# Performance work log

Hardware: AMD Instinct MI355X
Metric: run time of the kernel (lower is better)

Reference implementation:

```python
import jax, jax.numpy as jnp
import numpy as np

N = 100000      # points
M = 12500       # cluster centers
E0 = 1600000    # point-level edges
E1 = 400000     # cluster-level edges
F_IN = 4        # raw point feature dim (e.g. intensity + extras)
D = 64          # hidden feature width
N_CLASSES = 8


def setup_inputs() -> dict:
    key = jax.random.key(0)
    ks = jax.random.split(key, 20)
    s = 0.05
    d = {}
    d["features"] = jax.random.normal(ks[0], (N, F_IN), jnp.float32)
    d["points"] = jax.random.normal(ks[1], (N, 3), jnp.float32)
    d["cluster_centers"] = jax.random.normal(ks[2], (M, 3), jnp.float32)
    d["l0_edges"] = jax.random.randint(ks[3], (E0, 2), 0, N)
    d["l1_edges"] = jax.random.randint(ks[4], (E1, 2), 0, M)
    d["labels"] = jax.random.randint(ks[5], (N,), 0, M)
    # Feature_extract MLP
    d["W_fe"] = s * jax.random.normal(ks[6], (F_IN + 3, D), jnp.float32)
    d["b_fe"] = jnp.zeros((D,), jnp.float32)
    # 4 Mini_GNN layers (layer2, layer2_1, layer6, layer6_1), stacked
    d["mini_We"] = s * jax.random.normal(ks[7], (4, D + 3, D), jnp.float32)
    d["mini_be"] = jnp.zeros((4, D), jnp.float32)
    d["mini_Wu"] = s * jax.random.normal(ks[8], (4, D, D), jnp.float32)
    d["mini_bu"] = jnp.zeros((4, D), jnp.float32)
    # Mini_to_Large
    d["W_m1"] = s * jax.random.normal(ks[9], (D + 3, D), jnp.float32)
    d["b_m1"] = jnp.zeros((D,), jnp.float32)
    d["W_m2"] = s * jax.random.normal(ks[10], (D, D), jnp.float32)
    d["b_m2"] = jnp.zeros((D,), jnp.float32)
    # 2 GNN layers on cluster graph (layer4, layer4_1), stacked
    d["gnn_We"] = s * jax.random.normal(ks[11], (2, D + 3, D), jnp.float32)
    d["gnn_be"] = jnp.zeros((2, D), jnp.float32)
    d["gnn_Wu"] = s * jax.random.normal(ks[12], (2, D, D), jnp.float32)
    d["gnn_bu"] = jnp.zeros((2, D), jnp.float32)
    # Large_to_Mini
    d["W_l"] = s * jax.random.normal(ks[13], (D + 3, D), jnp.float32)
    d["b_l"] = jnp.zeros((D,), jnp.float32)
    # Classifier
    d["W_c"] = s * jax.random.normal(ks[14], (D, N_CLASSES), jnp.float32)
    d["b_c"] = jnp.zeros((N_CLASSES,), jnp.float32)
    return d


def _gnn_layer(feat, pos, edges, We, be, Wu, bu, n_nodes):
    """PointGNN-style layer: gather -> edge MLP -> scatter max -> update MLP -> residual."""
    src, dst = edges[:, 0], edges[:, 1]
    e_in = jnp.concatenate([pos[src] - pos[dst], feat[src]], axis=-1)  # [E, 3+D]
    h = jax.nn.relu(e_in @ We + be)                                     # [E, D]
    agg = jax.ops.segment_max(h, dst, num_segments=n_nodes)            # [n, D]
    agg = jnp.where(jnp.isneginf(agg), 0.0, agg)  # nodes with no in-edges -> 0
    return jax.nn.relu(agg @ Wu + bu) + feat


def reference(features, points, cluster_centers, l0_edges, l1_edges, labels,
              W_fe, b_fe, mini_We, mini_be, mini_Wu, mini_bu,
              W_m1, b_m1, W_m2, b_m2, gnn_We, gnn_be, gnn_Wu, gnn_bu,
              W_l, b_l, W_c, b_c):
    rel = points - cluster_centers[labels]  # [N, 3] point pos relative to its cluster
    # layer1: Feature_extract
    f1 = jax.nn.relu(jnp.concatenate([features, rel], -1) @ W_fe + b_fe)
    # layer2 / layer2_1: Mini_GNN (scatter max) on point graph
    f2 = _gnn_layer(f1, points, l0_edges, mini_We[0], mini_be[0], mini_Wu[0], mini_bu[0], N)
    f2_1 = _gnn_layer(f2, points, l0_edges, mini_We[1], mini_be[1], mini_Wu[1], mini_bu[1], N)
    # layer3: Mini_to_Large (scatter sum by labels)
    h = jax.nn.relu(jnp.concatenate([f2_1, rel], -1) @ W_m1 + b_m1)
    c = jax.ops.segment_sum(h, labels, num_segments=M)  # [M, D]
    f3 = jax.nn.relu(c @ W_m2 + b_m2)
    # layer4 / layer4_1: GNN (scatter max) on cluster graph
    f4 = _gnn_layer(f3, cluster_centers, l1_edges, gnn_We[0], gnn_be[0], gnn_Wu[0], gnn_bu[0], M)
    f4_1 = _gnn_layer(f4, cluster_centers, l1_edges, gnn_We[1], gnn_be[1], gnn_Wu[1], gnn_bu[1], M)
    # layer5: Large_to_Mini (gather by labels)
    f5 = jax.nn.relu(jnp.concatenate([f4_1[labels], rel], -1) @ W_l + b_l)
    # layer6 / layer6_1 with residual skips per call()
    f6 = _gnn_layer(f5, points, l0_edges, mini_We[2], mini_be[2], mini_Wu[2], mini_bu[2], N)
    f6 = f6 + f2_1
    f6_1 = _gnn_layer(f6, points, l0_edges, mini_We[3], mini_be[3], mini_Wu[3], mini_bu[3], N)
    final = f6_1 + f2
    return final @ W_c + b_c  # [N, N_CLASSES] per-point logits
```

## Files before the change

### kernel.cpp

```cpp
#include <hip/hip_runtime.h>


#define N_PTS   100000
#define M_CL    12500
#define E0_N    1600000
#define E1_N    400000

#define NB      256
#define BIN_CAP 16
#define RANGE0  391
#define RANGE1  49
#define BCAP0   8192
#define BCAP1   2048
#define BCAPL   1024

#define LSTR    72

typedef unsigned short ushortT;
typedef short  short8 __attribute__((ext_vector_type(8)));
typedef short  s4v    __attribute__((ext_vector_type(4)));
typedef float  v4f    __attribute__((ext_vector_type(4)));
typedef _Float16 h2   __attribute__((ext_vector_type(2)));
typedef unsigned u4v  __attribute__((ext_vector_type(4)));

__device__ inline ushortT f2bf(float x){
  union{float f; unsigned u;} v; v.f = x;
  unsigned r = v.u + 0x7fffu + ((v.u >> 16) & 1u);
  return (ushortT)(r >> 16);
}
__device__ inline float bf2f(ushortT h){
  union{unsigned u; float f;} v; v.u = ((unsigned)h) << 16;
  return v.f;
}
__device__ inline ushortT f2h(float x){
  union{_Float16 h; ushortT u;} v; v.h = (_Float16)x;
  return v.u;
}
__device__ inline float h2f(ushortT u){
  union{ushortT u; _Float16 h;} v; v.u = u;
  return (float)v.h;
}
__device__ inline h2 pkmax(h2 a, h2 b){ return __builtin_elementwise_max(a, b); }
__device__ inline h2 u2h(unsigned u){ union{unsigned u; h2 h;} v{u}; return v.h; }


struct WSrc { const float* p[22]; };

__global__ __launch_bounds__(256) void k_init_wprep(WSrc s, ushortT* __restrict__ wt, ushortT* __restrict__ wtc,
                                                    float* __restrict__ wpp,
                                                    int* c0, int* c1, int* cL){
  int blk = blockIdx.x;
  if (blk == 0){
    int t = threadIdx.x;
    c0[t] = t*BCAP0; c1[t] = t*BCAP1; cL[t] = t*BCAPL;
    return;
  }
  int slot = blk - 1;
  if (slot < 15){
    const float* src = s.p[slot];
    ushortT* dst = wt + slot*4096;
    for (int e=threadIdx.x; e<4096; e+=256){
      int nn = e>>6, p = e&63;
      int kk = (p&3)*16 + (p>>2);
      dst[e] = f2bf(src[kk*64+nn]);
    }
  } else if (slot == 15){
    const float* src = s.p[15];
    for (int e=threadIdx.x; e<1024; e+=256){
      int nn = e>>6, p = e&63;
      int kk = (p&3)*16 + (p>>2);
      wtc[e] = (nn<8) ? f2bf(src[kk*8+nn]) : (ushortT)0;
    }
  } else {
    for (int e=threadIdx.x; e<6*192; e+=256){
      int i = e/192, rem = e - i*192, r = rem>>6, p = rem&63;
      wpp[e] = s.p[16+i][r*64 + ((p&3)*16 + (p>>2))];
    }
  }
}


template<int RANGE, bool LAB>
__device__ void bin_seg(const int* __restrict__ edges, int E,
                        int* __restrict__ bcur, unsigned* __restrict__ tmp,
                        int bid, int nblk,
                        unsigned* stage, int* scnt, int* sbase){
  int tid = threadIdx.x;
  int nchunks = (E + 2047) / 2048;
  for (int c = bid; c < nchunks; c += nblk){
    int base = c*2048;
    scnt[tid] = 0;
    __syncthreads();
    #pragma unroll
    for (int r=0;r<8;++r){
      int e = base + r*256 + tid;
      if (e < E){
        int s, d;
        if (LAB){ s = e; d = edges[e]; }
        else    { int2 ed = ((const int2*)edges)[e]; s = ed.x; d = ed.y; }
        int bk = d / RANGE;
        unsigned packed = ((unsigned)s << 11) | (unsigned)(d - bk*RANGE);
        int pos = atomicAdd(&scnt[bk], 1);
        if (pos < BIN_CAP) stage[bk*BIN_CAP+pos] = packed;
        else tmp[atomicAdd(&bcur[bk],1)] = packed;
      }
    }
    __syncthreads();
    {
      int nfl = scnt[tid]; if (nfl > BIN_CAP) nfl = BIN_CAP;
      sbase[tid] = atomicAdd(&bcur[tid], nfl);
    }
    __syncthreads();
    int wv = tid >> 6, ln = tid & 63;
    for (int bb=0; bb<16; ++bb){
      int bk = wv*64 + bb*4 + (ln>>4);
      int ent = ln & 15;
      int nf = scnt[bk]; if (nf > BIN_CAP) nf = BIN_CAP;
      if (ent < nf) tmp[sbase[bk]+ent] = stage[bk*BIN_CAP+ent];
    }
    __syncthreads();
  }
}

template<int RANGE, int BCAP, int K>
__device__ void csr_build_seg(const unsigned* __restrict__ tmp, const int* __restrict__ bcur,
                              int n, int* __restrict__ offs, int* __restrict__ csr,
                              int b, int* hist, int* part){
  int tid = threadIdx.x;
  int dlo = b*RANGE;
  int range = n - dlo; if (range > RANGE) range = RANGE; if (range < 0) range = 0;
  int cnt = bcur[b] - b*BCAP;
  part[tid] = bcur[tid] - tid*BCAP;
  __syncthreads();
  for (int st=1; st<256; st<<=1){
    int x = (tid >= st) ? part[tid-st] : 0;
    __syncthreads();
    part[tid] += x;
    __syncthreads();
  }
  int gb = part[b] - cnt;
  int total = part[NB-1];
  if (b == NB-1 && tid == 0) offs[n] = total;
  __syncthreads();
  for (int t=tid; t<RANGE; t+=256) hist[t] = 0;
  __syncthreads();
  const unsigned* sl = tmp + (size_t)b*BCAP;
  for (int j=tid; j<cnt; j+=256) atomicAdd(&hist[sl[j] & 2047u], 1);
  __syncthreads();
  int s = 0; int loc[K];
  #pragma unroll
  for (int kk=0; kk<K; ++kk){
    int idx = tid*K + kk;
    int v = (idx < RANGE) ? hist[idx] : 0;
    loc[kk] = s; s += v;
  }
  part[tid] = s; __syncthreads();
  int own = s;
  for (int st=1; st<256; st<<=1){
    int x = (tid >= st) ? part[tid-st] : 0;
    __syncthreads();
    part[tid] += x;
    __syncthreads();
  }
  int ebase = part[tid] - own;
  __syncthreads();
  #pragma unroll
  for (int kk=0; kk<K; ++kk){
    int idx = tid*K + kk;
    if (idx < RANGE){
      int ex = ebase + loc[kk];
      if (idx < range) offs[dlo+idx] = gb + ex;
      hist[idx] = ex;
    }
  }
  __syncthreads();
  for (int j=tid; j<cnt; j+=256){
    unsigned p = sl[j];
    int pos = atomicAdd(&hist[p & 2047u], 1);
    csr[gb + pos] = (int)(p >> 11);
  }
}

__global__ __launch_bounds__(256) void k_build_all(
    const unsigned* t0, const int* bc0, int* offs0, int* csr0,
    const unsigned* t1, const int* bc1, int* offs1, int* csr1,
    const unsigned* tL, const int* bcL, int* offsL, int* csrL){
  __shared__ int hist[RANGE0];
  __shared__ int part[256];
  int b = blockIdx.x;
  if (b < 256)      csr_build_seg<RANGE0,BCAP0,2>(t0, bc0, N_PTS, offs0, csr0, b, hist, part);
  else if (b < 512) csr_build_seg<RANGE1,BCAP1,1>(t1, bc1, M_CL, offs1, csr1, b-256, hist, part);
  else              csr_build_seg<RANGE1,BCAPL,1>(tL, bcL, M_CL, offsL, csrL, b-512, hist, part);
}


__global__ __launch_bounds__(256) void k_bin_f1g(
    const int* __restrict__ l0e, const int* __restrict__ l1e, const int* __restrict__ labels,
    int* bc0, int* bc1, int* bcL,
    unsigned* t0, unsigned* t1, unsigned* tL,
    const float* __restrict__ features, const float* __restrict__ points,
    const float* __restrict__ centers,
    const float* __restrict__ W, const float* __restrict__ bfe,
    const ushortT* __restrict__ Wt2, const float* __restrict__ bias2,
    const float* __restrict__ Wr2,
    float* __restrict__ rel, ushortT* __restrict__ f1b,
    ushortT* __restrict__ gout, int n, int ntiles, int nf1blk)
{
  __shared__ char smem[18432];
  int b = blockIdx.x;
  if (b < 1027){
    unsigned* stage = (unsigned*)smem;
    int* scnt = (int*)(smem + 16384);
    int* sbase = (int*)(smem + 17408);
    if (b < 782)      bin_seg<RANGE0,false>(l0e, E0_N, bc0, t0, b, 782, stage, scnt, sbase);
    else if (b < 978) bin_seg<RANGE1,false>(l1e, E1_N, bc1, t1, b-782, 196, stage, scnt, sbase);
    else              bin_seg<RANGE1,true >(labels, N_PTS, bcL, tL, b-978, 49, stage, scnt, sbase);
    return;
  }
  ushortT* lds = (ushortT*)smem;
  int bb = b - 1027;
  int tid = threadIdx.x;
  int lane = tid & 63, wslot = tid >> 6;
  int quad = lane >> 4, l15 = lane & 15;
  int permL = (lane & 15)*4 + (lane >> 4);
  int r3 = lane/3, c3 = lane - r3*3;
  int gw = (bb*256 + tid) >> 6;
  int nw = (nf1blk*256) >> 6;
  float Wf0=W[0*64+lane], Wf1=W[1*64+lane], Wf2=W[2*64+lane], Wf3=W[3*64+lane];
  float wr0=W[4*64+lane], wr1=W[5*64+lane], wr2=W[6*64+lane];
  float bias=bfe[lane];
  short8 s0_0 = *(const short8*)(Wt2 + ( 0 + l15)*64 +  0 + quad*8);
  short8 s0_1 = *(const short8*)(Wt2 + ( 0 + l15)*64 + 32 + quad*8);
  short8 s1_0 = *(const short8*)(Wt2 + (16 + l15)*64 +  0 + quad*8);
  short8 s1_1 = *(const short8*)(Wt2 + (16 + l15)*64 + 32 + quad*8);
  short8 s2_0 = *(const short8*)(Wt2 + (32 + l15)*64 +  0 + quad*8);
  short8 s2_1 = *(const short8*)(Wt2 + (32 + l15)*64 + 32 + quad*8);
  short8 s3_0 = *(const short8*)(Wt2 + (48 + l15)*64 +  0 + quad*8);
  short8 s3_1 = *(const short8*)(Wt2 + (48 + l15)*64 + 32 + quad*8);
  float eb0 = bias2[l15], eb1 = bias2[16+l15], eb2 = bias2[32+l15], eb3 = bias2[48+l15];
  float e0c0=Wr2[0*64+l15], e0c1=Wr2[0*64+16+l15], e0c2=Wr2[0*64+32+l15], e0c3=Wr2[0*64+48+l15];
  float e1c0=Wr2[1*64+l15], e1c1=Wr2[1*64+16+l15], e1c2=Wr2[1*64+32+l15], e1c3=Wr2[1*64+48+l15];
  float e2c0=Wr2[2*64+l15], e2c1=Wr2[2*64+16+l15], e2c2=Wr2[2*64+32+l15], e2c3=Wr2[2*64+48+l15];

  for (int t=gw; t<ntiles; t+=nw){
    int i0 = t*16;
    int lab16 = labels[min(i0 + (lane & 15), n-1)];
    float fv  = features[(size_t)min(i0 + (lane>>2), n-1)*4 + (lane & 3)];
    int lb = __shfl(lab16, (r3 < 16) ? r3 : 0, 64);
    float pv = 0.f, relv = 0.f;
    if (lane < 48){
      int rowp = i0 + r3;
      int rc = (rowp < n) ? rowp : (n-1);
      pv = points[(size_t)rc*3 + c3];
      float cv = centers[(size_t)lb*3 + c3];
      relv = pv - cv;
      if (rowp < n) rel[(size_t)rowp*3 + c3] = relv;
    }
    #pragma unroll
    for (int r=0;r<16;++r){
      float rx = __shfl(relv, 3*r+0, 64);
      float ry = __shfl(relv, 3*r+1, 64);
      float rz = __shfl(relv, 3*r+2, 64);
      float f0 = __shfl(fv, 4*r+0, 64);
      float f1 = __shfl(fv, 4*r+1, 64);
      float f2 = __shfl(fv, 4*r+2, 64);
      float f3 = __shfl(fv, 4*r+3, 64);
      float acc = bias + wr0*rx + wr1*ry + wr2*rz;
      acc += f0*Wf0 + f1*Wf1;
      acc += f2*Wf2 + f3*Wf3;
      acc = fmaxf(acc, 0.f);
      ushortT ab = f2bf(acc);
      int row = i0 + r;
      if (row < n) f1b[(size_t)row*64 + permL] = ab;
      lds[wslot*(16*LSTR) + r*LSTR + permL] = ab;
    }
    __builtin_amdgcn_wave_barrier();
    const ushortT* lp = lds + wslot*(16*LSTR) + l15*LSTR + quad*8;
    short8 sa0 = *(const short8*)(lp);
    short8 sa1 = *(const short8*)(lp + 32);
    __builtin_amdgcn_wave_barrier();
    v4f ec0 = {0.f,0.f,0.f,0.f}, ec1 = ec0, ec2 = ec0, ec3 = ec0;
    ec0 = __builtin_amdgcn_mfma_f32_16x16x32_bf16(sa0, s0_0, ec0, 0,0,0);
    ec1 = __builtin_amdgcn_mfma_f32_16x16x32_bf16(sa0, s1_0, ec1, 0,0,0);
    ec2 = __builtin_amdgcn_mfma_f32_16x16x32_bf16(sa0, s2_0, ec2, 0,0,0);
    ec3 = __builtin_amdgcn_mfma_f32_16x16x32_bf16(sa0, s3_0, ec3, 0,0,0);
    ec0 = __builtin_amdgcn_mfma_f32_16x16x32_bf16(sa1, s0_1, ec0, 0,0,0);
    ec1 = __builtin_amdgcn_mfma_f32_16x16x32_bf16(sa1, s1_1, ec1, 0,0,0);
    ec2 = __builtin_amdgcn_mfma_f32_16x16x32_bf16(sa1, s2_1, ec2, 0,0,0);
    ec3 = __builtin_amdgcn_mfma_f32_16x16x32_bf16(sa1, s3_1, ec3, 0,0,0);
    #pragma unroll
    for (int r=0;r<4;++r){
      int row = i0 + quad*4 + r;
      if (row < n){
        int rr4 = quad*4 + r;
        float vx = __shfl(pv, 3*rr4+0, 64);
        float vy = __shfl(pv, 3*rr4+1, 64);
        float vz = __shfl(pv, 3*rr4+2, 64);
        float g0 = ec0[r] + eb0 + vx*e0c0 + vy*e1c0 + vz*e2c0;
        float g1 = ec1[r] + eb1 + vx*e0c1 + vy*e1c1 + vz*e2c1;
        float g2 = ec2[r] + eb2 + vx*e0c2 + vy*e1c2 + vz*e2c2;
        float g3 = ec3[r] + eb3 + vx*e0c3 + vy*e1c3 + vz*e2c3;
        s4v o; o.x=(short)f2h(g0); o.y=(short)f2h(g1); o.z=(short)f2h(g2); o.w=(short)f2h(g3);
        *(s4v*)(gout + (size_t)row*64 + l15*4) = o;
      }
    }
  }
}


template<bool RELU, int NRES, bool USEREL, bool GATHER, bool OUT16, bool F16O, int EMODE, bool ERELU>
__global__ __launch_bounds__(256) void k_gemm(
    const ushortT* __restrict__ A, const ushortT* __restrict__ Wt,
    const float* __restrict__ bias, const float* __restrict__ Wr,
    const float* __restrict__ rel, const int* __restrict__ gidx,
    const ushortT* __restrict__ r1, const ushortT* __restrict__ r2,
    ushortT* __restrict__ out16,
    const ushortT* __restrict__ Wt2, const float* __restrict__ bias2,
    const float* __restrict__ Wr2, const float* __restrict__ vec2,
    void* __restrict__ eout,
    int n, int ntiles)
{
  constexpr int LDSZ = (EMODE>0) ? 4*16*LSTR : 4;
  __shared__ ushortT lds[LDSZ];
  int tid = threadIdx.x;
  int lane = tid & 63, wslot = tid >> 6;
  int quad = lane >> 4, l15 = lane & 15;
  int r3 = lane/3, c3 = lane - r3*3;
  int gw = (blockIdx.x*256 + tid) >> 6;
  int nw = (gridDim.x*256) >> 6;

  short8 bfr0_0 = *(const short8*)(Wt + ( 0 + l15)*64 +  0 + quad*8);
  short8 bfr0_1 = *(const short8*)(Wt + ( 0 + l15)*64 + 32 + quad*8);
  short8 bfr1_0 = *(const short8*)(Wt + (16 + l15)*64 +  0 + quad*8);
  short8 bfr1_1 = *(const short8*)(Wt + (16 + l15)*64 + 32 + quad*8);
  short8 bfr2_0 = *(const short8*)(Wt + (32 + l15)*64 +  0 + quad*8);
  short8 bfr2_1 = *(const short8*)(Wt + (32 + l15)*64 + 32 + quad*8);
  short8 bfr3_0 = *(const short8*)(Wt + (48 + l15)*64 +  0 + quad*8);
  short8 bfr3_1 = *(const short8*)(Wt + (48 + l15)*64 + 32 + quad*8);
  float bs0 = bias[ 0 + l15], bs1 = bias[16 + l15];
  float bs2 = bias[32 + l15], bs3 = bias[48 + l15];
  float w0c0=0,w0c1=0,w0c2=0,w0c3=0, w1c0=0,w1c1=0,w1c2=0,w1c3=0, w2c0=0,w2c1=0,w2c2=0,w2c3=0;
  if (USEREL){
    w0c0=Wr[0*64+l15]; w0c1=Wr[0*64+16+l15]; w0c2=Wr[0*64+32+l15]; w0c3=Wr[0*64+48+l15];
    w1c0=Wr[1*64+l15]; w1c1=Wr[1*64+16+l15]; w1c2=Wr[1*64+32+l15]; w1c3=Wr[1*64+48+l15];
    w2c0=Wr[2*64+l15]; w2c1=Wr[2*64+16+l15]; w2c2=Wr[2*64+32+l15]; w2c3=Wr[2*64+48+l15];
  }

  short8 s0_0{}, s0_1{}, s1_0{}, s1_1{}, s2_0{}, s2_1{}, s3_0{}, s3_1{};
  float eb0=0, eb1=0, eb2=0, eb3=0;
  float e0c0=0,e0c1=0,e0c2=0,e0c3=0, e1c0=0,e1c1=0,e1c2=0,e1c3=0, e2c0=0,e2c1=0,e2c2=0,e2c3=0;
  float ebias_c = 0.f;
  if (EMODE == 1){
    s0_0 = *(const short8*)(Wt2 + ( 0 + l15)*64 +  0 + quad*8);
    s0_1 = *(const short8*)(Wt2 + ( 0 + l15)*64 + 32 + quad*8);
    s1_0 = *(const short8*)(Wt2 + (16 + l15)*64 +  0 + quad*8);
    s1_1 = *(const short8*)(Wt2 + (16 + l15)*64 + 32 + quad*8);
    s2_0 = *(const short8*)(Wt2 + (32 + l15)*64 +  0 + quad*8);
    s2_1 = *(const short8*)(Wt2 + (32 + l15)*64 + 32 + quad*8);
    s3_0 = *(const short8*)(Wt2 + (48 + l15)*64 +  0 + quad*8);
    s3_1 = *(const short8*)(Wt2 + (48 + l15)*64 + 32 + quad*8);
    eb0 = bias2[l15]; eb1 = bias2[16+l15]; eb2 = bias2[32+l15]; eb3 = bias2[48+l15];
    e0c0=Wr2[0*64+l15]; e0c1=Wr2[0*64+16+l15]; e0c2=Wr2[0*64+32+l15]; e0c3=Wr2[0*64+48+l15];
    e1c0=Wr2[1*64+l15]; e1c1=Wr2[1*64+16+l15]; e1c2=Wr2[1*64+32+l15]; e1c3=Wr2[1*64+48+l15];
    e2c0=Wr2[2*64+l15]; e2c1=Wr2[2*64+16+l15]; e2c2=Wr2[2*64+32+l15]; e2c3=Wr2[2*64+48+l15];
  } else if (EMODE == 2){
    s0_0 = *(const short8*)(Wt2 + l15*64 +  0 + quad*8);
    s0_1 = *(const short8*)(Wt2 + l15*64 + 32 + quad*8);
    ebias_c = (l15 < 8) ? bias2[l15] : 0.f;
  }

  for (int t=gw; t<ntiles; t+=nw){
    int i0 = t*16;
    int rowA = i0 + l15; if (rowA >= n) rowA = n-1;
    if (GATHER) rowA = gidx[rowA];
    const ushortT* ap = A + (size_t)rowA*64 + quad*8;
    short8 a0 = *(const short8*)(ap);
    short8 a1 = *(const short8*)(ap + 32);
    float relL = 0.f;
    if (USEREL && lane < 48){
      int rc = i0 + r3; if (rc >= n) rc = n-1;
      relL = rel[(size_t)rc*3 + c3];
    }
    v4f ac0 = {0.f,0.f,0.f,0.f}, ac1 = ac0, ac2 = ac0, ac3 = ac0;
    ac0 = __builtin_amdgcn_mfma_f32_16x16x32_bf16(a0, bfr0_0, ac0, 0,0,0);
    ac1 = __builtin_amdgcn_mfma_f32_16x16x32_bf16(a0, bfr1_0, ac1, 0,0,0);
    ac2 = __builtin_amdgcn_mfma_f32_16x16x32_bf16(a0, bfr2_0, ac2, 0,0,0);
    ac3 = __builtin_amdgcn_mfma_f32_16x16x32_bf16(a0, bfr3_0, ac3, 0,0,0);
    ac0 = __builtin_amdgcn_mfma_f32_16x16x32_bf16(a1, bfr0_1, ac0, 0,0,0);
    ac1 = __builtin_amdgcn_mfma_f32_16x16x32_bf16(a1, bfr1_1, ac1, 0,0,0);
    ac2 = __builtin_amdgcn_mfma_f32_16x16x32_bf16(a1, bfr2_1, ac2, 0,0,0);
    ac3 = __builtin_amdgcn_mfma_f32_16x16x32_bf16(a1, bfr3_1, ac3, 0,0,0);

    #pragma unroll
    for (int r=0;r<4;++r){
      int row = i0 + quad*4 + r;
      bool rowok = (row < n);
      float v0 = ac0[r] + bs0, v1 = ac1[r] + bs1, v2 = ac2[r] + bs2, v3 = ac3[r] + bs3;
      if (USEREL){
        int rr4 = quad*4 + r;
        float rx = __shfl(relL, 3*rr4+0, 64);
        float ry = __shfl(relL, 3*rr4+1, 64);
        float rz = __shfl(relL, 3*rr4+2, 64);
        v0 += rx*w0c0 + ry*w1c0 + rz*w2c0;
        v1 += rx*w0c1 + ry*w1c1 + rz*w2c1;
        v2 += rx*w0c2 + ry*w1c2 + rz*w2c2;
        v3 += rx*w0c3 + ry*w1c3 + rz*w2c3;
      }
      if (RELU){ v0=fmaxf(v0,0.f); v1=fmaxf(v1,0.f); v2=fmaxf(v2,0.f); v3=fmaxf(v3,0.f); }
      size_t pb = (size_t)row*64 + l15*4;
      if (rowok){
        if (NRES>=1){
          s4v rv = *(const s4v*)(r1 + pb);
          v0 += bf2f((ushortT)rv.x); v1 += bf2f((ushortT)rv.y);
          v2 += bf2f((ushortT)rv.z); v3 += bf2f((ushortT)rv.w);
        }
        if (NRES>=2){
          s4v rv = *(const s4v*)(r2 + pb);
          v0 += bf2f((ushortT)rv.x); v1 += bf2f((ushortT)rv.y);
          v2 += bf2f((ushortT)rv.z); v3 += bf2f((ushortT)rv.w);
        }
        if (OUT16){
          s4v o;
          if (F16O){ o.x=(short)f2h(v0); o.y=(short)f2h(v1); o.z=(short)f2h(v2); o.w=(short)f2h(v3); }
          else     { o.x=(short)f2bf(v0); o.y=(short)f2bf(v1); o.z=(short)f2bf(v2); o.w=(short)f2bf(v3); }
          *(s4v*)(out16 + pb) = o;
        }
      }
      if (EMODE > 0){
        int lb = wslot*(16*LSTR) + (quad*4+r)*LSTR + l15*4;
        s4v o; o.x=(short)f2bf(v0); o.y=(short)f2bf(v1); o.z=(short)f2bf(v2); o.w=(short)f2bf(v3);
        *(s4v*)(lds + lb) = o;
      }
    }

    if (EMODE > 0){
      __builtin_amdgcn_wave_barrier();
      const ushortT* lp = lds + wslot*(16*LSTR) + l15*LSTR + quad*8;
      short8 sa0 = *(const short8*)(lp);
      short8 sa1 = *(const short8*)(lp + 32);
      __builtin_amdgcn_wave_barrier();
      if (EMODE == 1){
        float posv = 0.f;
        if (lane < 48){
          int rc = i0 + r3; if (rc >= n) rc = n-1;
          posv = vec2[(size_t)rc*3 + c3];
        }
        v4f ec0 = {0.f,0.f,0.f,0.f}, ec1 = ec0, ec2 = ec0, ec3 = ec0;
        ec0 = __builtin_amdgcn_mfma_f32_16x16x32_bf16(sa0, s0_0, ec0, 0,0,0);
        ec1 = __builtin_amdgcn_mfma_f32_16x16x32_bf16(sa0, s1_0, ec1, 0,0,0);
        ec2 = __builtin_amdgcn_mfma_f32_16x16x32_bf16(sa0, s2_0, ec2, 0,0,0);
        ec3 = __builtin_amdgcn_mfma_f32_16x16x32_bf16(sa0, s3_0, ec3, 0,0,0);
        ec0 = __builtin_amdgcn_mfma_f32_16x16x32_bf16(sa1, s0_1, ec0, 0,0,0);
        ec1 = __builtin_amdgcn_mfma_f32_16x16x32_bf16(sa1, s1_1, ec1, 0,0,0);
        ec2 = __builtin_amdgcn_mfma_f32_16x16x32_bf16(sa1, s2_1, ec2, 0,0,0);
        ec3 = __builtin_amdgcn_mfma_f32_16x16x32_bf16(sa1, s3_1, ec3, 0,0,0);
        ushortT* eo = (ushortT*)eout;
        #pragma unroll
        for (int r=0;r<4;++r){
          int row = i0 + quad*4 + r;
          if (row < n){
            int rr4 = quad*4 + r;
            float vx = __shfl(posv, 3*rr4+0, 64);
            float vy = __shfl(posv, 3*rr4+1, 64);
            float vz = __shfl(posv, 3*rr4+2, 64);
            float g0 = ec0[r] + eb0 + vx*e0c0 + vy*e1c0 + vz*e2c0;
            float g1 = ec1[r] + eb1 + vx*e0c1 + vy*e1c1 + vz*e2c1;
            float g2 = ec2[r] + eb2 + vx*e0c2 + vy*e1c2 + vz*e2c2;
            float g3 = ec3[r] + eb3 + vx*e0c3 + vy*e1c3 + vz*e2c3;
            if (ERELU){ g0=fmaxf(g0,0.f); g1=fmaxf(g1,0.f); g2=fmaxf(g2,0.f); g3=fmaxf(g3,0.f); }
            s4v o; o.x=(short)f2h(g0); o.y=(short)f2h(g1); o.z=(short)f2h(g2); o.w=(short)f2h(g3);
            *(s4v*)(eo + (size_t)row*64 + l15*4) = o;
          }
        }
      } else {
        v4f ec = {0.f,0.f,0.f,0.f};
        ec = __builtin_amdgcn_mfma_f32_16x16x32_bf16(sa0, s0_0, ec, 0,0,0);
        ec = __builtin_amdgcn_mfma_f32_16x16x32_bf16(sa1, s0_1, ec, 0,0,0);
        if (l15 < 8){
          float* eo = (float*)eout;
          #pragma unroll
          for (int r=0;r<4;++r){
            int row = i0 + quad*4 + r;
            if (row < n) eo[(size_t)row*8 + l15] = ec[r] + ebias_c;
          }
        }
      }
    }
  }
}


__global__ __launch_bounds__(256) void k_edge_agg(const int* __restrict__ offs, const int* __restrict__ csr,
                                                  const float* __restrict__ pos, const ushortT* __restrict__ g,
                                                  const float* __restrict__ Wp, ushortT* __restrict__ agg, int n){
  int lane = threadIdx.x & 63;
  int grp = lane >> 3, d8 = lane & 7;
  int gbase = lane & 56;
  int gw = (blockIdx.x*256 + threadIdx.x) >> 6;
  int nw = (gridDim.x*256) >> 6;
  const u4v* g4 = (const u4v*)g;
  float2 w0[4], w1[4], w2[4];
  #pragma unroll
  for (int q=0;q<4;++q){
    w0[q] = *(const float2*)(Wp + 0*64 + d8*8 + 2*q);
    w1[q] = *(const float2*)(Wp + 1*64 + d8*8 + 2*q);
    w2[q] = *(const float2*)(Wp + 2*64 + d8*8 + 2*q);
  }
  const h2 NEGBIG = {(_Float16)-60000.f, (_Float16)-60000.f};
  int n8 = (n+7) >> 3;
  for (int ii=gw; ii<n8; ii+=nw){
    int i0 = ii*8;
    int ig = i0 + grp; bool ok = ig < n; if (!ok) ig = n-1;
    int b = offs[ig], e = offs[ig+1];
    int cnt = e - b, c1 = cnt - 1;
    int mx = cnt;
    mx = max(mx, __shfl_xor(mx, 8, 64));
    mx = max(mx, __shfl_xor(mx, 16, 64));
    mx = max(mx, __shfl_xor(mx, 32, 64));
    h2 m0=NEGBIG, m1=NEGBIG, m2=NEGBIG, m3=NEGBIG;
    for (int J=0; J<mx; J+=8){
      if (J < cnt){
        int sv = csr[b + min(J + d8, c1)];
        #pragma unroll
        for (int jj=0; jj<8; ++jj){
          int s = __shfl(sv, gbase + jj, 64);
          u4v u = g4[(size_t)s*8 + d8];
          m0 = pkmax(m0, u2h(u.x));
          m1 = pkmax(m1, u2h(u.y));
          m2 = pkmax(m2, u2h(u.z));
          m3 = pkmax(m3, u2h(u.w));
        }
      }
    }
    float px = pos[ig*3+0], py = pos[ig*3+1], pz = pos[ig*3+2];
    u4v outv;
    {
      float sA = w0[0].x*px + w1[0].x*py + w2[0].x*pz;
      float sB = w0[0].y*px + w1[0].y*py + w2[0].y*pz;
      outv.x = (unsigned)f2bf(fmaxf((float)m0.x - sA, 0.f)) |
               ((unsigned)f2bf(fmaxf((float)m0.y - sB, 0.f)) << 16);
    }
    {
      float sA = w0[1].x*px + w1[1].x*py + w2[1].x*pz;
      float sB = w0[1].y*px + w1[1].y*py + w2[1].y*pz;
      outv.y = (unsigned)f2bf(fmaxf((float)m1.x - sA, 0.f)) |
               ((unsigned)f2bf(fmaxf((float)m1.y - sB, 0.f)) << 16);
    }
    {
      float sA = w0[2].x*px + w1[2].x*py + w2[2].x*pz;
      float sB = w0[2].y*px + w1[2].y*py + w2[2].y*pz;
      outv.z = (unsigned)f2bf(fmaxf((float)m2.x - sA, 0.f)) |
               ((unsigned)f2bf(fmaxf((float)m2.y - sB, 0.f)) << 16);
    }
    {
      float sA = w0[3].x*px + w1[3].x*py + w2[3].x*pz;
      float sB = w0[3].y*px + w1[3].y*py + w2[3].y*pz;
      outv.w = (unsigned)f2bf(fmaxf((float)m3.x - sA, 0.f)) |
               ((unsigned)f2bf(fmaxf((float)m3.y - sB, 0.f)) << 16);
    }
    if (ok) ((u4v*)agg)[(size_t)ig*8 + d8] = outv;
  }
}


__global__ __launch_bounds__(256) void k_seg_gather(const int* __restrict__ offs, const int* __restrict__ csr,
                                                    const ushortT* __restrict__ h, ushortT* __restrict__ c, int m){
  int lane = threadIdx.x & 63;
  int wv = (blockIdx.x*256 + threadIdx.x) >> 6;
  if (wv >= m) return;
  int b = offs[wv], e = offs[wv+1];
  float acc = 0.f;
  for (int k=b; k<e; ++k){
    int i = csr[k];
    acc += h2f(h[(size_t)i*64+lane]);
  }
  c[(size_t)wv*64+lane] = f2bf(acc);
}


extern "C" void kernel_launch(void* const* d_in, const int* in_sizes, int n_in,
                              void* d_out, int out_size, void* d_ws, size_t ws_size,
                              hipStream_t stream){
  const float* features = (const float*)d_in[0];
  const float* points   = (const float*)d_in[1];
  const float* centers  = (const float*)d_in[2];
  const int*   l0e      = (const int*)d_in[3];
  const int*   l1e      = (const int*)d_in[4];
  const int*   labels   = (const int*)d_in[5];
  const float* W_fe = (const float*)d_in[6];
  const float* b_fe = (const float*)d_in[7];
  const float* mWe  = (const float*)d_in[8];
  const float* mbe  = (const float*)d_in[9];
  const float* mWu  = (const float*)d_in[10];
  const float* mbu  = (const float*)d_in[11];
  const float* W_m1 = (const float*)d_in[12];
  const float* b_m1 = (const float*)d_in[13];
  const float* W_m2 = (const float*)d_in[14];
  const float* b_m2 = (const float*)d_in[15];
  const float* gWe  = (const float*)d_in[16];
  const float* gbe  = (const float*)d_in[17];
  const float* gWu  = (const float*)d_in[18];
  const float* gbu  = (const float*)d_in[19];
  const float* W_l  = (const float*)d_in[20];
  const float* b_l  = (const float*)d_in[21];
  const float* W_c  = (const float*)d_in[22];
  const float* b_c  = (const float*)d_in[23];
  float* out = (float*)d_out;

  char* w = (char*)d_ws;
  size_t off = 0;
  auto alloc = [&](size_t bytes)->void*{
    void* p = (void*)(w + off);
    off = (off + bytes + 255) & ~(size_t)255;
    return p;
  };
  float* rel  = (float*)alloc((size_t)N_PTS*3*4);
  ushortT* UF1 = (ushortT*)alloc((size_t)N_PTS*64*2);
  ushortT* UF2 = (ushortT*)alloc((size_t)N_PTS*64*2);
  ushortT* UF21= (ushortT*)alloc((size_t)N_PTS*64*2);
  ushortT* UF5 = (ushortT*)alloc((size_t)N_PTS*64*2);
  ushortT* UF6 = (ushortT*)alloc((size_t)N_PTS*64*2);
  ushortT* gbuf= (ushortT*)alloc((size_t)N_PTS*64*2);
  ushortT* abuf= (ushortT*)alloc((size_t)N_PTS*64*2);
  ushortT* cb_b= (ushortT*)alloc((size_t)M_CL*64*2);
  ushortT* UF3 = (ushortT*)alloc((size_t)M_CL*64*2);
  ushortT* UF4 = (ushortT*)alloc((size_t)M_CL*64*2);
  ushortT* cg_b= (ushortT*)alloc((size_t)M_CL*64*2);
  ushortT* cagg_b = (ushortT*)alloc((size_t)M_CL*64*2);
  ushortT* f41_b  = (ushortT*)alloc((size_t)M_CL*64*2);
  ushortT* wt  = (ushortT*)alloc((size_t)15*4096*2);
  ushortT* wtc = (ushortT*)alloc((size_t)1024*2);
  float* wpp = (float*)alloc((size_t)6*192*4);
  int* offs0 = (int*)alloc((size_t)(N_PTS+1)*4);
  int* csr0  = (int*)alloc((size_t)E0_N*4);
  int* offs1 = (int*)alloc((size_t)(M_CL+1)*4);
  int* csr1  = (int*)alloc((size_t)E1_N*4);
  int* offsL = (int*)alloc((size_t)(M_CL+1)*4);
  int* csrL  = (int*)alloc((size_t)N_PTS*4);
  unsigned* tmp0 = (unsigned*)alloc((size_t)NB*BCAP0*4);
  unsigned* tmp1 = (unsigned*)alloc((size_t)NB*BCAP1*4);
  unsigned* tmpL = (unsigned*)alloc((size_t)NB*BCAPL*4);
  int* bcur0 = (int*)alloc(NB*4);
  int* bcur1 = (int*)alloc(NB*4);
  int* bcurL = (int*)alloc(NB*4);
  (void)ws_size; (void)in_sizes; (void)n_in; (void)out_size;

  const int NT_N = (N_PTS+15)/16;
  const int NT_M = (M_CL +15)/16;
  const int GBG_N = 1563;
  const int GBG_M = 196;
  const int GB_N  = 3125;
  const int GB_BIN = 1027;

  WSrc ws{};
  ws.p[0]=mWu+0*4096; ws.p[1]=mWu+1*4096; ws.p[2]=mWu+2*4096; ws.p[3]=mWu+3*4096;
  ws.p[4]=W_m2; ws.p[5]=gWu+0*4096; ws.p[6]=gWu+1*4096;
  ws.p[7]=mWe+0*4288+192; ws.p[8]=mWe+1*4288+192; ws.p[9]=mWe+2*4288+192; ws.p[10]=mWe+3*4288+192;
  ws.p[11]=W_m1; ws.p[12]=W_l; ws.p[13]=gWe+0*4288+192; ws.p[14]=gWe+1*4288+192;
  ws.p[15]=W_c;
  ws.p[16]=mWe+0*4288; ws.p[17]=mWe+1*4288; ws.p[18]=mWe+2*4288; ws.p[19]=mWe+3*4288;
  ws.p[20]=gWe+0*4288; ws.p[21]=gWe+1*4288;
  k_init_wprep<<<18, 256, 0, stream>>>(ws, wt, wtc, wpp, bcur0, bcur1, bcurL);
  k_bin_f1g<<<GB_BIN + GBG_N, 256, 0, stream>>>(l0e, l1e, labels, bcur0, bcur1, bcurL, tmp0, tmp1, tmpL,
      features, points, centers, W_fe, b_fe,
      wt+7*4096, mbe+0, mWe+0*4288, rel, UF1, gbuf, N_PTS, NT_N, GBG_N);
  k_build_all<<<768, 256, 0, stream>>>(tmp0, bcur0, offs0, csr0,
                                       tmp1, bcur1, offs1, csr1,
                                       tmpL, bcurL, offsL, csrL);

  k_edge_agg<<<GB_N,256,0,stream>>>(offs0, csr0, points, gbuf, wpp+0*192, abuf, N_PTS);
  k_gemm<true,1,false,false,true,false,1,false><<<GBG_N,256,0,stream>>>(abuf, wt+0*4096, mbu+0,
      nullptr, nullptr, nullptr, UF1, nullptr, UF2,
      wt+8*4096, mbe+64, mWe+1*4288, points, gbuf, N_PTS, NT_N);
  k_edge_agg<<<GB_N,256,0,stream>>>(offs0, csr0, points, gbuf, wpp+1*192, abuf, N_PTS);
  k_gemm<true,1,false,false,true,false,1,true><<<GBG_N,256,0,stream>>>(abuf, wt+1*4096, mbu+64,
      nullptr, nullptr, nullptr, UF2, nullptr, UF21,
      wt+11*4096, b_m1, W_m1+4096, rel, gbuf, N_PTS, NT_N);
  k_seg_gather<<<(M_CL*64+255)/256, 256, 0, stream>>>(offsL, csrL, gbuf, cb_b, M_CL);
  k_gemm<true,0,false,false,true,false,1,false><<<GBG_M,256,0,stream>>>(cb_b, wt+4*4096, b_m2,
      nullptr, nullptr, nullptr, nullptr, nullptr, UF3,
      wt+13*4096, gbe+0, gWe+0*4288, centers, cg_b, M_CL, NT_M);
  k_edge_agg<<<GBG_M,256,0,stream>>>(offs1, csr1, centers, cg_b, wpp+4*192, cagg_b, M_CL);
  k_gemm<true,1,false,false,true,false,1,false><<<GBG_M,256,0,stream>>>(cagg_b, wt+5*4096, gbu+0,
      nullptr, nullptr, nullptr, UF3, nullptr, UF4,
      wt+14*4096, gbe+64, gWe+1*4288, centers, cg_b, M_CL, NT_M);
  k_edge_agg<<<GBG_M,256,0,stream>>>(offs1, csr1, centers, cg_b, wpp+5*192, cagg_b, M_CL);
  k_gemm<true,1,false,false,true,false,0,false><<<GBG_M,256,0,stream>>>(cagg_b, wt+6*4096, gbu+64,
      nullptr, nullptr, nullptr, UF4, nullptr, f41_b,
      nullptr, nullptr, nullptr, nullptr, nullptr, M_CL, NT_M);
  k_gemm<true,0,true,true,true,false,1,false><<<GBG_N,256,0,stream>>>(f41_b, wt+12*4096, b_l,
      W_l+4096, rel, labels, nullptr, nullptr, UF5,
      wt+9*4096, mbe+128, mWe+2*4288, points, gbuf, N_PTS, NT_N);
  k_edge_agg<<<GB_N,256,0,stream>>>(offs0, csr0, points, gbuf, wpp+2*192, abuf, N_PTS);
  k_gemm<true,2,false,false,true,false,1,false><<<GBG_N,256,0,stream>>>(abuf, wt+2*4096, mbu+128,
      nullptr, nullptr, nullptr, UF5, UF21, UF6,
      wt+10*4096, mbe+192, mWe+3*4288, points, gbuf, N_PTS, NT_N);
  k_edge_agg<<<GB_N,256,0,stream>>>(offs0, csr0, points, gbuf, wpp+3*192, abuf, N_PTS);
  k_gemm<true,2,false,false,false,false,2,false><<<GBG_N,256,0,stream>>>(abuf, wt+3*4096, mbu+192,
      nullptr, nullptr, nullptr, UF6, UF2, nullptr,
      wtc, b_c, nullptr, nullptr, out, N_PTS, NT_N);
}
```

Measured before the change: 458.2 us.

## Replace atomic global binning with per-chunk local sort and gather-based CSR build

```diff
diff --git a/kernel.cpp b/kernel.cpp
--- a/kernel.cpp
+++ b/kernel.cpp
@@ -7,12 +7,14 @@
 #define E1_N    400000
 
 #define NB      256
-#define BIN_CAP 16
 #define RANGE0  391
 #define RANGE1  49
-#define BCAP0   8192
-#define BCAP1   2048
-#define BCAPL   1024
+#define NCH0    782
+#define NCH1    196
+#define NCHL    49
+#define CAP0    7168
+#define CAP1    2048
+#define CAPL    768
 
 #define LSTR    72
 
@@ -48,11 +50,11 @@
 
 __global__ __launch_bounds__(256) void k_init_wprep(WSrc s, ushortT* __restrict__ wt, ushortT* __restrict__ wtc,
                                                     float* __restrict__ wpp,
-                                                    int* c0, int* c1, int* cL){
+                                                    int* b0, int* b1, int* bL){
   int blk = blockIdx.x;
   if (blk == 0){
     int t = threadIdx.x;
-    c0[t] = t*BCAP0; c1[t] = t*BCAP1; cL[t] = t*BCAPL;
+    b0[t] = 0; b1[t] = 0; bL[t] = 0;
     return;
   }
   int slot = blk - 1;
@@ -81,56 +83,70 @@
 
 
 template<int RANGE, bool LAB>
-__device__ void bin_seg(const int* __restrict__ edges, int E,
-                        int* __restrict__ bcur, unsigned* __restrict__ tmp,
-                        int bid, int nblk,
-                        unsigned* stage, int* scnt, int* sbase){
+__device__ void sort_chunk(const int* __restrict__ edges, int E, int c,
+                           unsigned* __restrict__ slab, int* __restrict__ offC,
+                           int* __restrict__ btot,
+                           unsigned* slds, int* hist, int* pfx){
   int tid = threadIdx.x;
-  int nchunks = (E + 2047) / 2048;
-  for (int c = bid; c < nchunks; c += nblk){
-    int base = c*2048;
-    scnt[tid] = 0;
+  int base = c*2048;
+  int cnt = E - base; if (cnt > 2048) cnt = 2048;
+  hist[tid] = 0;
+  __syncthreads();
+  int bk[8]; unsigned pk[8];
+  #pragma unroll
+  for (int r=0;r<8;++r){
+    int e = base + r*256 + tid;
+    bk[r] = -1; pk[r] = 0;
+    if (e < E){
+      int s, d;
+      if (LAB){ s = e; d = edges[e]; }
+      else    { int2 ed = ((const int2*)edges)[e]; s = ed.x; d = ed.y; }
+      int b = d / RANGE;
+      bk[r] = b;
+      pk[r] = ((unsigned)s << 11) | (unsigned)(d - b*RANGE);
+      atomicAdd(&hist[b], 1);
+    }
+  }
+  __syncthreads();
+  int own = hist[tid];
+  pfx[tid] = own;
+  __syncthreads();
+  for (int st=1; st<256; st<<=1){
+    int x = (tid >= st) ? pfx[tid-st] : 0;
     __syncthreads();
-    #pragma unroll
-    for (int r=0;r<8;++r){
-      int e = base + r*256 + tid;
-      if (e < E){
-        int s, d;
-        if (LAB){ s = e; d = edges[e]; }
-        else    { int2 ed = ((const int2*)edges)[e]; s = ed.x; d = ed.y; }
-        int bk = d / RANGE;
-        unsigned packed = ((unsigned)s << 11) | (unsigned)(d - bk*RANGE);
-        int pos = atomicAdd(&scnt[bk], 1);
-        if (pos < BIN_CAP) stage[bk*BIN_CAP+pos] = packed;
-        else tmp[atomicAdd(&bcur[bk],1)] = packed;
-      }
-    }
+    pfx[tid] += x;
     __syncthreads();
-    {
-      int nfl = scnt[tid]; if (nfl > BIN_CAP) nfl = BIN_CAP;
-      sbase[tid] = atomicAdd(&bcur[tid], nfl);
-    }
-    __syncthreads();
-    int wv = tid >> 6, ln = tid & 63;
-    for (int bb=0; bb<16; ++bb){
-      int bk = wv*64 + bb*4 + (ln>>4);
-      int ent = ln & 15;
-      int nf = scnt[bk]; if (nf > BIN_CAP) nf = BIN_CAP;
-      if (ent < nf) tmp[sbase[bk]+ent] = stage[bk*BIN_CAP+ent];
-    }
-    __syncthreads();
-  }
-}
-
-template<int RANGE, int BCAP, int K>
-__device__ void csr_build_seg(const unsigned* __restrict__ tmp, const int* __restrict__ bcur,
+  }
+  int excl = pfx[tid] - own;
+  offC[(size_t)c*257 + tid] = excl;
+  if (tid == 0) offC[(size_t)c*257 + 256] = cnt;
+  atomicAdd(&btot[tid], own);
+  hist[tid] = excl;
+  __syncthreads();
+  #pragma unroll
+  for (int r=0;r<8;++r){
+    if (bk[r] >= 0){
+      int pos = atomicAdd(&hist[bk[r]], 1);
+      slds[pos] = pk[r];
+    }
+  }
+  __syncthreads();
+  unsigned* sg = slab + (size_t)c*2048;
+  for (int i=tid; i<cnt; i+=256) sg[i] = slds[i];
+}
+
+
+template<int RANGE, int NCHUNK, int CAP, int K>
+__device__ void csr_build_seg(const unsigned* __restrict__ slab, const int* __restrict__ offC,
+                              const int* __restrict__ btot,
                               int n, int* __restrict__ offs, int* __restrict__ csr,
-                              int b, int* hist, int* part){
+                              int b, unsigned* stage, int* hist, int* part){
+  constexpr int CPT = (NCHUNK + 255) / 256;
   int tid = threadIdx.x;
   int dlo = b*RANGE;
   int range = n - dlo; if (range > RANGE) range = RANGE; if (range < 0) range = 0;
-  int cnt = bcur[b] - b*BCAP;
-  part[tid] = bcur[tid] - tid*BCAP;
+  int ownT = btot[tid];
+  part[tid] = ownT;
   __syncthreads();
   for (int st=1; st<256; st<<=1){
     int x = (tid >= st) ? part[tid-st] : 0;
@@ -138,14 +154,46 @@
     part[tid] += x;
     __syncthreads();
   }
-  int gb = part[b] - cnt;
+  int gb = part[b] - btot[b];
   int total = part[NB-1];
   if (b == NB-1 && tid == 0) offs[n] = total;
+  int cnt = btot[b];
+  __syncthreads();
+  int mst[CPT], mlen[CPT];
+  int csum = 0;
+  #pragma unroll
+  for (int k=0;k<CPT;++k){
+    int c = tid + k*256;
+    int l = 0, s0 = 0;
+    if (c < NCHUNK){
+      s0 = offC[(size_t)c*257 + b];
+      l  = offC[(size_t)c*257 + b + 1] - s0;
+    }
+    mst[k] = s0; mlen[k] = l; csum += l;
+  }
+  part[tid] = csum;
+  __syncthreads();
+  int own2 = csum;
+  for (int st=1; st<256; st<<=1){
+    int x = (tid >= st) ? part[tid-st] : 0;
+    __syncthreads();
+    part[tid] += x;
+    __syncthreads();
+  }
+  int sb = part[tid] - own2;
+  #pragma unroll
+  for (int k=0;k<CPT;++k){
+    int c = tid + k*256;
+    if (c < NCHUNK){
+      const unsigned* sg = slab + (size_t)c*2048 + mst[k];
+      for (int j=0;j<mlen[k];++j) stage[sb+j] = sg[j];
+      sb += mlen[k];
+    }
+  }
   __syncthreads();
   for (int t=tid; t<RANGE; t+=256) hist[t] = 0;
   __syncthreads();
-  const unsigned* sl = tmp + (size_t)b*BCAP;
-  for (int j=tid; j<cnt; j+=256) atomicAdd(&hist[sl[j] & 2047u], 1);
+  for (int j=tid; j<cnt; j+=256) atomicAdd(&hist[stage[j] & 2047u], 1);
   __syncthreads();
   int s = 0; int loc[K];
   #pragma unroll
@@ -155,14 +203,14 @@
     loc[kk] = s; s += v;
   }
   part[tid] = s; __syncthreads();
-  int own = s;
+  int own3 = s;
   for (int st=1; st<256; st<<=1){
     int x = (tid >= st) ? part[tid-st] : 0;
     __syncthreads();
     part[tid] += x;
     __syncthreads();
   }
-  int ebase = part[tid] - own;
+  int ebase = part[tid] - own3;
   __syncthreads();
   #pragma unroll
   for (int kk=0; kk<K; ++kk){
@@ -175,29 +223,31 @@
   }
   __syncthreads();
   for (int j=tid; j<cnt; j+=256){
-    unsigned p = sl[j];
+    unsigned p = stage[j];
     int pos = atomicAdd(&hist[p & 2047u], 1);
     csr[gb + pos] = (int)(p >> 11);
   }
 }
 
 __global__ __launch_bounds__(256) void k_build_all(
-    const unsigned* t0, const int* bc0, int* offs0, int* csr0,
-    const unsigned* t1, const int* bc1, int* offs1, int* csr1,
-    const unsigned* tL, const int* bcL, int* offsL, int* csrL){
+    const unsigned* s0, const int* oc0, const int* bt0, int* offs0, int* csr0,
+    const unsigned* s1, const int* oc1, const int* bt1, int* offs1, int* csr1,
+    const unsigned* sL, const int* ocL, const int* btL, int* offsL, int* csrL){
+  __shared__ unsigned stage[CAP0];
   __shared__ int hist[RANGE0];
   __shared__ int part[256];
   int b = blockIdx.x;
-  if (b < 256)      csr_build_seg<RANGE0,BCAP0,2>(t0, bc0, N_PTS, offs0, csr0, b, hist, part);
-  else if (b < 512) csr_build_seg<RANGE1,BCAP1,1>(t1, bc1, M_CL, offs1, csr1, b-256, hist, part);
-  else              csr_build_seg<RANGE1,BCAPL,1>(tL, bcL, M_CL, offsL, csrL, b-512, hist, part);
+  if (b < 256)      csr_build_seg<RANGE0,NCH0,CAP0,2>(s0, oc0, bt0, N_PTS, offs0, csr0, b, stage, hist, part);
+  else if (b < 512) csr_build_seg<RANGE1,NCH1,CAP1,1>(s1, oc1, bt1, M_CL, offs1, csr1, b-256, stage, hist, part);
+  else              csr_build_seg<RANGE1,NCHL,CAPL,1>(sL, ocL, btL, M_CL, offsL, csrL, b-512, stage, hist, part);
 }
 
 
 __global__ __launch_bounds__(256) void k_bin_f1g(
     const int* __restrict__ l0e, const int* __restrict__ l1e, const int* __restrict__ labels,
-    int* bc0, int* bc1, int* bcL,
-    unsigned* t0, unsigned* t1, unsigned* tL,
+    int* bt0, int* bt1, int* btL,
+    unsigned* s0, unsigned* s1, unsigned* sL,
+    int* oc0, int* oc1, int* ocL,
     const float* __restrict__ features, const float* __restrict__ points,
     const float* __restrict__ centers,
     const float* __restrict__ W, const float* __restrict__ bfe,
@@ -206,15 +256,15 @@
     float* __restrict__ rel, ushortT* __restrict__ f1b,
     ushortT* __restrict__ gout, int n, int ntiles, int nf1blk)
 {
-  __shared__ char smem[18432];
+  __shared__ char smem[10240];
   int b = blockIdx.x;
   if (b < 1027){
-    unsigned* stage = (unsigned*)smem;
-    int* scnt = (int*)(smem + 16384);
-    int* sbase = (int*)(smem + 17408);
-    if (b < 782)      bin_seg<RANGE0,false>(l0e, E0_N, bc0, t0, b, 782, stage, scnt, sbase);
-    else if (b < 978) bin_seg<RANGE1,false>(l1e, E1_N, bc1, t1, b-782, 196, stage, scnt, sbase);
-    else              bin_seg<RANGE1,true >(labels, N_PTS, bcL, tL, b-978, 49, stage, scnt, sbase);
+    unsigned* slds = (unsigned*)smem;
+    int* hist = (int*)(smem + 8192);
+    int* pfx  = (int*)(smem + 9216);
+    if (b < 782)      sort_chunk<RANGE0,false>(l0e, E0_N, b,     s0, oc0, bt0, slds, hist, pfx);
+    else if (b < 978) sort_chunk<RANGE1,false>(l1e, E1_N, b-782, s1, oc1, bt1, slds, hist, pfx);
+    else              sort_chunk<RANGE1,true >(labels, N_PTS, b-978, sL, ocL, btL, slds, hist, pfx);
     return;
   }
   ushortT* lds = (ushortT*)smem;
@@ -637,12 +687,15 @@
   int* csr1  = (int*)alloc((size_t)E1_N*4);
   int* offsL = (int*)alloc((size_t)(M_CL+1)*4);
   int* csrL  = (int*)alloc((size_t)N_PTS*4);
-  unsigned* tmp0 = (unsigned*)alloc((size_t)NB*BCAP0*4);
-  unsigned* tmp1 = (unsigned*)alloc((size_t)NB*BCAP1*4);
-  unsigned* tmpL = (unsigned*)alloc((size_t)NB*BCAPL*4);
-  int* bcur0 = (int*)alloc(NB*4);
-  int* bcur1 = (int*)alloc(NB*4);
-  int* bcurL = (int*)alloc(NB*4);
+  unsigned* slab0 = (unsigned*)alloc((size_t)NCH0*2048*4);
+  unsigned* slab1 = (unsigned*)alloc((size_t)NCH1*2048*4);
+  unsigned* slabL = (unsigned*)alloc((size_t)NCHL*2048*4);
+  int* offC0 = (int*)alloc((size_t)NCH0*257*4);
+  int* offC1 = (int*)alloc((size_t)NCH1*257*4);
+  int* offCL = (int*)alloc((size_t)NCHL*257*4);
+  int* btot0 = (int*)alloc(NB*4);
+  int* btot1 = (int*)alloc(NB*4);
+  int* btotL = (int*)alloc(NB*4);
   (void)ws_size; (void)in_sizes; (void)n_in; (void)out_size;
 
   const int NT_N = (N_PTS+15)/16;
@@ -660,13 +713,14 @@
   ws.p[15]=W_c;
   ws.p[16]=mWe+0*4288; ws.p[17]=mWe+1*4288; ws.p[18]=mWe+2*4288; ws.p[19]=mWe+3*4288;
   ws.p[20]=gWe+0*4288; ws.p[21]=gWe+1*4288;
-  k_init_wprep<<<18, 256, 0, stream>>>(ws, wt, wtc, wpp, bcur0, bcur1, bcurL);
-  k_bin_f1g<<<GB_BIN + GBG_N, 256, 0, stream>>>(l0e, l1e, labels, bcur0, bcur1, bcurL, tmp0, tmp1, tmpL,
+  k_init_wprep<<<18, 256, 0, stream>>>(ws, wt, wtc, wpp, btot0, btot1, btotL);
+  k_bin_f1g<<<GB_BIN + GBG_N, 256, 0, stream>>>(l0e, l1e, labels, btot0, btot1, btotL,
+      slab0, slab1, slabL, offC0, offC1, offCL,
       features, points, centers, W_fe, b_fe,
       wt+7*4096, mbe+0, mWe+0*4288, rel, UF1, gbuf, N_PTS, NT_N, GBG_N);
-  k_build_all<<<768, 256, 0, stream>>>(tmp0, bcur0, offs0, csr0,
-                                       tmp1, bcur1, offs1, csr1,
-                                       tmpL, bcurL, offsL, csrL);
+  k_build_all<<<768, 256, 0, stream>>>(slab0, offC0, btot0, offs0, csr0,
+                                       slab1, offC1, btot1, offs1, csr1,
+                                       slabL, offCL, btotL, offsL, csrL);
 
   k_edge_agg<<<GB_N,256,0,stream>>>(offs0, csr0, points, gbuf, wpp+0*192, abuf, N_PTS);
   k_gemm<true,1,false,false,true,false,1,false><<<GBG_N,256,0,stream>>>(abuf, wt+0*4096, mbu+0,
```

Result: no change. 462.3 us (+0.9%).
